# Optimization experiments

Measured on AMD Instinct MI355X. Metric: run time of the kernel, lower is better.

Reference implementation:

```python
import jax, jax.numpy as jnp
import numpy as np

N_ATOMS = 50000
N_EDGES = 500000
N_BASIS = 128
N_FILTERS = 128
N_GAUSS = 50
N_CONV = 3
CUTOFF = 5.0
MOL_SIZE = 1000


def ssp(x):
    # shifted softplus: softplus(x) - log(2)
    return jax.nn.softplus(x) - jnp.log(2.0).astype(x.dtype)


def setup_inputs() -> dict:
    key = jax.random.key(0)
    ks = jax.random.split(key, 24)

    r = jax.random.randint(ks[0], (N_ATOMS, 1), 1, 100)            # atomic numbers (0 is padding)
    xyz = jax.random.normal(ks[1], (N_ATOMS, 3)) * 3.0             # coordinates
    a = jax.random.randint(ks[2], (N_EDGES, 2), 0, N_ATOMS)        # edge list [E,2]

    embed = jax.random.normal(ks[3], (100, N_BASIS)) * 0.1
    embed = embed.at[0].set(0.0)                                   # padding_idx=0

    def w(k, fan_in, fan_out):
        return jax.random.normal(k, (fan_in, fan_out)) / jnp.sqrt(fan_in)

    def wl(k, fan_in, fan_out):  # stacked over N_CONV layers
        return jax.random.normal(k, (N_CONV, fan_in, fan_out)) / jnp.sqrt(fan_in)

    inp = {
        "r": r, "xyz": xyz, "a": a, "mol_size": MOL_SIZE,
        "embed": embed,
        # per-conv node filter Dense(B,F)
        "Wn": wl(ks[4], N_BASIS, N_FILTERS), "bn": jnp.zeros((N_CONV, N_FILTERS)),
        # per-conv edge filter Dense(G,G) -> ssp -> Dense(G,F)
        "We1": wl(ks[5], N_GAUSS, N_GAUSS), "be1": jnp.zeros((N_CONV, N_GAUSS)),
        "We2": wl(ks[6], N_GAUSS, N_FILTERS), "be2": jnp.zeros((N_CONV, N_FILTERS)),
        # per-conv update Dense(F,B) -> ssp -> Dense(B,B)
        "Wu1": wl(ks[7], N_FILTERS, N_BASIS), "bu1": jnp.zeros((N_CONV, N_BASIS)),
        "Wu2": wl(ks[8], N_BASIS, N_BASIS), "bu2": jnp.zeros((N_CONV, N_BASIS)),
        # readout
        "W1": w(ks[9], N_BASIS, N_BASIS // 2), "b1": jnp.zeros((N_BASIS // 2,)),
        "W2": w(ks[10], N_BASIS // 2, 1), "b2": jnp.zeros((1,)),
    }
    return inp


def reference(r, xyz, a, mol_size, embed, Wn, bn, We1, be1, We2, be2,
              Wu1, bu1, Wu2, bu2, W1, b1, W2, b2):
    n = xyz.shape[0]
    i, j = a[:, 0], a[:, 1]

    # per-edge distances [E,1]
    d = jnp.sqrt(jnp.sum((xyz[i] - xyz[j]) ** 2, axis=1, keepdims=True))

    # Gaussian smearing (fixed, non-trainable): offsets linspace(0, cutoff, G)
    offsets = jnp.linspace(0.0, CUTOFF, N_GAUSS)
    width = offsets[1] - offsets[0]
    coeff = -0.5 / (width ** 2)
    g = jnp.exp(coeff * (d - offsets[None, :]) ** 2)  # [E, G]

    # atom embedding [n, B]
    h = embed[r[:, 0]]

    for l in range(N_CONV):
        ef = ssp(g @ We1[l] + be1[l]) @ We2[l] + be2[l]          # [E, F] edge filter
        nodef = h @ Wn[l] + bn[l]                                # [n, F] node filter
        # symmetric message passing over undirected edge list
        agg = jax.ops.segment_sum(nodef[j] * ef, i, num_segments=n) \
            + jax.ops.segment_sum(nodef[i] * ef, j, num_segments=n)  # [n, F]
        dr = ssp(agg @ Wu1[l] + bu1[l]) @ Wu2[l] + bu2[l]        # [n, B]
        h = h + dr

    # atomwise readout
    e_atom = ssp(h @ W1 + b1) @ W2 + b2                          # [n, 1]

    # per-molecule pooling (equal-size molecules)
    seg = jnp.arange(n) // mol_size
    return jax.ops.segment_sum(e_atom, seg, num_segments=n // mol_size)  # [n_mols, 1]
```

## Files before the change

### kernel.cpp

```cpp
#include <hip/hip_runtime.h>
#include <hip/hip_bf16.h>

#define NG 50
#define NB 128

__device__ __forceinline__ float sspf(float x){
  float t = __expf(-fabsf(x));
  return fmaxf(x, 0.f) + __logf(1.f + t) - 0.6931471805599453094f;
}

constexpr float RBF_STEP  = 5.0f / 49.0f;
constexpr float RBF_COEFF = -0.5f / (RBF_STEP * RBF_STEP);

__global__ void embed_k(const int* __restrict__ r, const float* __restrict__ embed,
                        float* __restrict__ h, int N){
  int idx = blockIdx.x * blockDim.x + threadIdx.x;
  if (idx < N * 32){
    int n = idx >> 5, c = (idx & 31) * 4;
    *(float4*)&h[(size_t)n * NB + c] = *(const float4*)&embed[(size_t)r[n] * NB + c];
  }
}

__global__ void dist_k(const int* __restrict__ a, const float* __restrict__ xyz,
                       float* __restrict__ d, int E){
  int e = blockIdx.x * blockDim.x + threadIdx.x;
  if (e < E){
    int i = a[2*e], j = a[2*e+1];
    float dx = xyz[3*i+0] - xyz[3*j+0];
    float dy = xyz[3*i+1] - xyz[3*j+1];
    float dz = xyz[3*i+2] - xyz[3*j+2];
    d[e] = sqrtf(dx*dx + dy*dy + dz*dz);
  }
}

__global__ void hist_k(const int* __restrict__ a, int* __restrict__ cnt, int E){
  int e = blockIdx.x * blockDim.x + threadIdx.x;
  if (e < E){
    atomicAdd(&cnt[a[2*e]],   1);
    atomicAdd(&cnt[a[2*e+1]], 1);
  }
}

__global__ void pad_k(const int* __restrict__ cnt, int* __restrict__ pcnt, int N){
  int i = blockIdx.x*blockDim.x + threadIdx.x;
  if (i < N) pcnt[i] = (cnt[i] + 7) & ~7;
}

#define SCAN_TILE 512
__global__ void reduce_k(const int* __restrict__ cnt, int* __restrict__ bsum, int N){
  __shared__ int s[256];
  int b = blockIdx.x, t = threadIdx.x;
  int i0 = b*SCAN_TILE + t;
  int v = 0;
  if (i0 < N)       v += cnt[i0];
  if (i0+256 < N)   v += cnt[i0+256];
  s[t] = v; __syncthreads();
  for (int o=128;o>0;o>>=1){ if (t<o) s[t]+=s[t+o]; __syncthreads(); }
  if (t==0) bsum[b] = s[0];
}

__global__ void scanb_k(const int* __restrict__ bsum, int* __restrict__ boff, int nb){
  if (threadIdx.x==0 && blockIdx.x==0){
    int acc = 0;
    for (int i=0;i<nb;i++){ boff[i]=acc; acc+=bsum[i]; }
  }
}

__global__ void scan2_k(const int* __restrict__ cnt, const int* __restrict__ boff,
                        int* __restrict__ rowptr, int N, int total){
  __shared__ int s[256];
  int b = blockIdx.x, t = threadIdx.x;
  int i0 = b*SCAN_TILE;
  int a0 = (i0+2*t   < N) ? cnt[i0+2*t]   : 0;
  int a1 = (i0+2*t+1 < N) ? cnt[i0+2*t+1] : 0;
  int pair = a0 + a1;
  s[t] = pair; __syncthreads();
  for (int o=1;o<256;o<<=1){
    int v = (t>=o) ? s[t-o] : 0;
    __syncthreads();
    s[t] += v;
    __syncthreads();
  }
  int excl = s[t] - pair + boff[b];
  if (i0+2*t   < N) rowptr[i0+2*t]   = excl;
  if (i0+2*t+1 < N) rowptr[i0+2*t+1] = excl + a0;
  if (b==0 && t==0) rowptr[N] = total;
}

__global__ void copy_k(const int* __restrict__ src, int* __restrict__ dst, int n){
  int i = blockIdx.x*blockDim.x + threadIdx.x;
  if (i < n) dst[i] = src[i];
}

__global__ void fill_k(const int* __restrict__ a, int* __restrict__ cur,
                       int* __restrict__ asrc, int* __restrict__ aedg,
                       int* __restrict__ tgtv, int E){
  int e = blockIdx.x*blockDim.x + threadIdx.x;
  if (e < E){
    int i = a[2*e], j = a[2*e+1];
    int p = atomicAdd(&cur[i], 1);
    asrc[p] = j; aedg[p] = e; tgtv[p] = i;
    int q = atomicAdd(&cur[j], 1);
    asrc[q] = i; aedg[q] = e; tgtv[q] = j;
  }
}

template<int ACT, int RESID>
__launch_bounds__(128, 3)
__global__ void gemm128_k(const float* __restrict__ in, const float* __restrict__ W,
                          const float* __restrict__ bias, float* __restrict__ out, int N){
  __shared__ float As[32][64];
  __shared__ float Ws[32][128];
  int tid = threadIdx.x;
  int tc = tid & 15, tr = tid >> 4;
  int row0 = blockIdx.x * 64;
  int c0 = tc * 8;

  float bcol[8];
  {
    float4 b0 = *(const float4*)&bias[c0];
    float4 b1 = *(const float4*)&bias[c0+4];
    bcol[0]=b0.x; bcol[1]=b0.y; bcol[2]=b0.z; bcol[3]=b0.w;
    bcol[4]=b1.x; bcol[5]=b1.y; bcol[6]=b1.z; bcol[7]=b1.w;
  }
  float acc[8][8];
  #pragma unroll
  for (int r=0;r<8;r++)
    #pragma unroll
    for (int q=0;q<8;q++) acc[r][q] = bcol[q];

  for (int kc=0; kc<4; kc++){
    #pragma unroll
    for (int p=0;p<4;p++){
      int f = tid + 128*p;
      int rr = f >> 3, kq = f & 7;
      int grow = row0 + rr;
      float4 v = (grow < N) ? *(const float4*)&in[(size_t)grow*NB + kc*32 + kq*4]
                            : make_float4(0.f,0.f,0.f,0.f);
      As[kq*4+0][rr] = v.x; As[kq*4+1][rr] = v.y;
      As[kq*4+2][rr] = v.z; As[kq*4+3][rr] = v.w;
    }
    #pragma unroll
    for (int p=0;p<8;p++){
      int f = tid + 128*p;
      int wk = f >> 5, cq = f & 31;
      *(float4*)&Ws[wk][cq*4] = *(const float4*)&W[(size_t)(kc*32+wk)*NB + cq*4];
    }
    __syncthreads();
    #pragma unroll 4
    for (int k=0;k<32;k++){
      float4 a0 = *(const float4*)&As[k][tr*8];
      float4 a1 = *(const float4*)&As[k][tr*8+4];
      float4 w0 = *(const float4*)&Ws[k][c0];
      float4 w1 = *(const float4*)&Ws[k][c0+4];
      float av[8] = {a0.x,a0.y,a0.z,a0.w,a1.x,a1.y,a1.z,a1.w};
      float wv[8] = {w0.x,w0.y,w0.z,w0.w,w1.x,w1.y,w1.z,w1.w};
      #pragma unroll
      for (int r=0;r<8;r++)
        #pragma unroll
        for (int q=0;q<8;q++) acc[r][q] += av[r]*wv[q];
    }
    __syncthreads();
  }
  #pragma unroll
  for (int r=0;r<8;r++){
    int row = row0 + tr*8 + r;
    if (row < N){
      float v[8];
      #pragma unroll
      for (int q=0;q<8;q++) v[q] = (ACT==1) ? sspf(acc[r][q]) : acc[r][q];
      if (RESID){
        float4 o0 = *(const float4*)&out[(size_t)row*NB + c0];
        float4 o1 = *(const float4*)&out[(size_t)row*NB + c0+4];
        v[0]+=o0.x; v[1]+=o0.y; v[2]+=o0.z; v[3]+=o0.w;
        v[4]+=o1.x; v[5]+=o1.y; v[6]+=o1.z; v[7]+=o1.w;
      }
      *(float4*)&out[(size_t)row*NB + c0]   = make_float4(v[0],v[1],v[2],v[3]);
      *(float4*)&out[(size_t)row*NB + c0+4] = make_float4(v[4],v[5],v[6],v[7]);
    }
  }
}

__launch_bounds__(256, 2)
__global__ void visit2_k(const float* __restrict__ dists,
                         const int* __restrict__ asrc, const int* __restrict__ aedg,
                         const int* __restrict__ tgtv,
                         const float* __restrict__ nodef,
                         const float* __restrict__ We1, const float* __restrict__ be1,
                         const float* __restrict__ We2, const float* __restrict__ be2,
                         float* __restrict__ agg, int Vmax){
  __shared__ float We1s[NG][64];
  __shared__ float We2s[NG][NB];
  __shared__ float buf[NG][NB];
  __shared__ float be1s[64], be2s[NB];
  __shared__ float ds_[NB];
  __shared__ int   srcs[NB], tgts[NB];
  __shared__ int   tgt8[16];
  int tid = threadIdx.x;

  int vbase = blockIdx.x * NB;
  if (tid < NB){
    int p = vbase + tid;
    if (p < Vmax){
      srcs[tid] = asrc[p]; tgts[tid] = tgtv[p];
      ds_[tid]  = dists[aedg[p]];
    } else {
      srcs[tid] = 0; tgts[tid] = -1; ds_[tid] = 0.f;
    }
  }
  __syncthreads();
  if (tgts[0] < 0) return;

  for (int idx = tid; idx < NG*64; idx += 256){
    int m = idx >> 6, k = idx & 63;
    We1s[m][k] = (k < NG) ? We1[m*NG + k] : 0.f;
  }
  for (int idx = tid; idx < NG*NB; idx += 256)
    We2s[0][idx] = We2[idx];
  if (tid < 64)  be1s[tid] = (tid < NG) ? be1[tid] : 0.f;
  if (tid < NB)  be2s[tid] = be2[tid];
  if (tid < 16)  tgt8[tid] = tgts[tid*8];

  for (int idx = tid; idx < NG*NB; idx += 256){
    int m = idx >> 7, e = idx & 127;
    float t = ds_[e] - RBF_STEP * (float)m;
    buf[m][e] = __expf(RBF_COEFF * t * t);
  }
  __syncthreads();

  int te = tid >> 4, tk = tid & 15;
  int e0 = te * 8, k0 = tk * 4;

  float tacc[8][4];
  {
    float4 bv = *(const float4*)&be1s[k0];
    float bq[4] = {bv.x,bv.y,bv.z,bv.w};
    #pragma unroll
    for (int r=0;r<8;r++)
      #pragma unroll
      for (int q=0;q<4;q++) tacc[r][q] = bq[q];
  }
  #pragma unroll 2
  for (int m=0;m<NG;m++){
    float4 w  = *(const float4*)&We1s[m][k0];
    float4 g0 = *(const float4*)&buf[m][e0];
    float4 g1 = *(const float4*)&buf[m][e0+4];
    float ge[8] = {g0.x,g0.y,g0.z,g0.w,g1.x,g1.y,g1.z,g1.w};
    float wv[4] = {w.x,w.y,w.z,w.w};
    #pragma unroll
    for (int r=0;r<8;r++)
      #pragma unroll
      for (int q=0;q<4;q++) tacc[r][q] += ge[r]*wv[q];
  }
  __syncthreads();
  #pragma unroll
  for (int q=0;q<4;q++){
    int k = k0 + q;
    if (k < NG){
      float v[8];
      #pragma unroll
      for (int r=0;r<8;r++) v[r] = sspf(tacc[r][q]);
      *(float4*)&buf[k][e0]   = make_float4(v[0],v[1],v[2],v[3]);
      *(float4*)&buf[k][e0+4] = make_float4(v[4],v[5],v[6],v[7]);
    }
  }
  __syncthreads();

  int c0 = tk * 8;
  float acc[8][8];
  {
    float4 b0 = *(const float4*)&be2s[c0];
    float4 b1 = *(const float4*)&be2s[c0+4];
    float bq[8] = {b0.x,b0.y,b0.z,b0.w,b1.x,b1.y,b1.z,b1.w};
    #pragma unroll
    for (int r=0;r<8;r++)
      #pragma unroll
      for (int q=0;q<8;q++) acc[r][q] = bq[q];
  }
  #pragma unroll 2
  for (int k=0;k<NG;k++){
    float4 w0 = *(const float4*)&We2s[k][c0];
    float4 w1 = *(const float4*)&We2s[k][c0+4];
    float4 t0 = *(const float4*)&buf[k][e0];
    float4 t1 = *(const float4*)&buf[k][e0+4];
    float tv[8] = {t0.x,t0.y,t0.z,t0.w,t1.x,t1.y,t1.z,t1.w};
    float wv[8] = {w0.x,w0.y,w0.z,w0.w,w1.x,w1.y,w1.z,w1.w};
    #pragma unroll
    for (int r=0;r<8;r++)
      #pragma unroll
      for (int q=0;q<8;q++) acc[r][q] += tv[r]*wv[q];
  }
  __syncthreads();

  float run[8];
  #pragma unroll
  for (int q=0;q<8;q++) run[q] = 0.f;
  #pragma unroll
  for (int r=0;r<8;r++){
    int t = tgts[e0+r];
    int s = srcs[e0+r];
    float4 n0 = *(const float4*)&nodef[(size_t)s*NB + c0];
    float4 n1 = *(const float4*)&nodef[(size_t)s*NB + c0+4];
    float nv[8] = {n0.x,n0.y,n0.z,n0.w,n1.x,n1.y,n1.z,n1.w};
    if (t >= 0){
      #pragma unroll
      for (int q=0;q<8;q++) run[q] += acc[r][q] * nv[q];
    }
  }
  float* part = &buf[0][0];
  #pragma unroll
  for (int q=0;q<8;q++) part[te*NB + c0 + q] = run[q];
  __syncthreads();

  int g = te;
  int t = tgt8[g];
  if (t >= 0 && (g == 0 || tgt8[g-1] != t)){
    int gend = g;
    while (gend+1 < 16 && tgt8[gend+1] == t) gend++;
    float s[8];
    #pragma unroll
    for (int q=0;q<8;q++) s[q] = 0.f;
    for (int g2=g; g2<=gend; ++g2)
      #pragma unroll
      for (int q=0;q<8;q++) s[q] += part[g2*NB + c0 + q];
    float* ap = &agg[(size_t)t*NB + c0];
    bool border = (g == 0) || (gend == 15);
    if (border){
      #pragma unroll
      for (int q=0;q<8;q++) atomicAdd(ap+q, s[q]);
    } else {
      *(float4*)ap     = make_float4(s[0],s[1],s[2],s[3]);
      *(float4*)(ap+4) = make_float4(s[4],s[5],s[6],s[7]);
    }
  }
}

__launch_bounds__(256, 2)
__global__ void visit_k(const float* __restrict__ dists,
                        const int* __restrict__ asrc, const int* __restrict__ aedg,
                        const int* __restrict__ tgtv,
                        const float* __restrict__ nodef,
                        const float* __restrict__ We1, const float* __restrict__ be1,
                        const float* __restrict__ We2, const float* __restrict__ be2,
                        float* __restrict__ agg, int V){
  __shared__ float We1s[NG][64];
  __shared__ float We2s[NG][NB];
  __shared__ float buf[NG][NB];
  __shared__ float be1s[64], be2s[NB];
  __shared__ float ds_[NB];
  __shared__ int   srcs[NB], tgts[NB];
  int tid = threadIdx.x;

  for (int idx = tid; idx < NG*64; idx += 256){
    int m = idx >> 6, k = idx & 63;
    We1s[m][k] = (k < NG) ? We1[m*NG + k] : 0.f;
  }
  for (int idx = tid; idx < NG*NB; idx += 256)
    We2s[0][idx] = We2[idx];
  if (tid < 64)  be1s[tid] = (tid < NG) ? be1[tid] : 0.f;
  if (tid < NB)  be2s[tid] = be2[tid];

  int vbase = blockIdx.x * NB;
  if (tid < NB){
    int p = vbase + tid;
    if (p < V){
      srcs[tid] = asrc[p]; tgts[tid] = tgtv[p];
      ds_[tid]  = dists[aedg[p]];
    } else {
      srcs[tid] = 0; tgts[tid] = -1; ds_[tid] = 0.f;
    }
  }
  __syncthreads();
  for (int idx = tid; idx < NG*NB; idx += 256){
    int m = idx >> 7, e = idx & 127;
    float t = ds_[e] - RBF_STEP * (float)m;
    buf[m][e] = __expf(RBF_COEFF * t * t);
  }
  __syncthreads();
  int te = tid >> 4, tk = tid & 15;
  int e0 = te * 8, k0 = tk * 4;
  float tacc[8][4];
  {
    float4 bv = *(const float4*)&be1s[k0];
    float bq[4] = {bv.x,bv.y,bv.z,bv.w};
    #pragma unroll
    for (int r=0;r<8;r++)
      #pragma unroll
      for (int q=0;q<4;q++) tacc[r][q] = bq[q];
  }
  #pragma unroll 2
  for (int m=0;m<NG;m++){
    float4 w  = *(const float4*)&We1s[m][k0];
    float4 g0 = *(const float4*)&buf[m][e0];
    float4 g1 = *(const float4*)&buf[m][e0+4];
    float ge[8] = {g0.x,g0.y,g0.z,g0.w,g1.x,g1.y,g1.z,g1.w};
    float wv[4] = {w.x,w.y,w.z,w.w};
    #pragma unroll
    for (int r=0;r<8;r++)
      #pragma unroll
      for (int q=0;q<4;q++) tacc[r][q] += ge[r]*wv[q];
  }
  __syncthreads();
  #pragma unroll
  for (int q=0;q<4;q++){
    int k = k0 + q;
    if (k < NG){
      float v[8];
      #pragma unroll
      for (int r=0;r<8;r++) v[r] = sspf(tacc[r][q]);
      *(float4*)&buf[k][e0]   = make_float4(v[0],v[1],v[2],v[3]);
      *(float4*)&buf[k][e0+4] = make_float4(v[4],v[5],v[6],v[7]);
    }
  }
  __syncthreads();
  int c0 = tk * 8;
  float acc[8][8];
  {
    float4 b0 = *(const float4*)&be2s[c0];
    float4 b1 = *(const float4*)&be2s[c0+4];
    float bq[8] = {b0.x,b0.y,b0.z,b0.w,b1.x,b1.y,b1.z,b1.w};
    #pragma unroll
    for (int r=0;r<8;r++)
      #pragma unroll
      for (int q=0;q<8;q++) acc[r][q] = bq[q];
  }
  #pragma unroll 2
  for (int k=0;k<NG;k++){
    float4 w0 = *(const float4*)&We2s[k][c0];
    float4 w1 = *(const float4*)&We2s[k][c0+4];
    float4 t0 = *(const float4*)&buf[k][e0];
    float4 t1 = *(const float4*)&buf[k][e0+4];
    float tv[8] = {t0.x,t0.y,t0.z,t0.w,t1.x,t1.y,t1.z,t1.w};
    float wv[8] = {w0.x,w0.y,w0.z,w0.w,w1.x,w1.y,w1.z,w1.w};
    #pragma unroll
    for (int r=0;r<8;r++)
      #pragma unroll
      for (int q=0;q<8;q++) acc[r][q] += tv[r]*wv[q];
  }
  int   curtgt = tgts[e0];
  float run[8];
  #pragma unroll
  for (int q=0;q<8;q++) run[q] = 0.f;
  #pragma unroll
  for (int r=0;r<8;r++){
    int t = tgts[e0+r];
    int s = srcs[e0+r];
    float4 n0 = *(const float4*)&nodef[(size_t)s*NB + c0];
    float4 n1 = *(const float4*)&nodef[(size_t)s*NB + c0+4];
    float nv[8] = {n0.x,n0.y,n0.z,n0.w,n1.x,n1.y,n1.z,n1.w};
    if (t != curtgt){
      if (curtgt >= 0){
        float* ap = &agg[(size_t)curtgt*NB + c0];
        #pragma unroll
        for (int q=0;q<8;q++) atomicAdd(ap+q, run[q]);
      }
      curtgt = t;
      #pragma unroll
      for (int q=0;q<8;q++) run[q] = 0.f;
    }
    if (t >= 0){
      #pragma unroll
      for (int q=0;q<8;q++) run[q] += acc[r][q] * nv[q];
    }
  }
  if (curtgt >= 0){
    float* ap = &agg[(size_t)curtgt*NB + c0];
    #pragma unroll
    for (int q=0;q<8;q++) atomicAdd(ap+q, run[q]);
  }
}

__launch_bounds__(256, 2)
__global__ void edge_k(const float* __restrict__ dists, const int* __restrict__ a,
                       const float* __restrict__ nodef,
                       const float* __restrict__ We1, const float* __restrict__ be1,
                       const float* __restrict__ We2, const float* __restrict__ be2,
                       float* __restrict__ agg, int E){
  __shared__ float We1s[NG][64];
  __shared__ float We2s[NG][NB];
  __shared__ float buf[NG][NB];
  __shared__ float be1s[64], be2s[NB];
  __shared__ float ds_[NB];
  __shared__ int   ijs[2*NB];
  int tid = threadIdx.x;

  for (int idx = tid; idx < NG*64; idx += 256){
    int m = idx >> 6, k = idx & 63;
    We1s[m][k] = (k < NG) ? We1[m*NG + k] : 0.f;
  }
  for (int idx = tid; idx < NG*NB; idx += 256)
    We2s[0][idx] = We2[idx];
  if (tid < 64)  be1s[tid] = (tid < NG) ? be1[tid] : 0.f;
  if (tid < NB)  be2s[tid] = be2[tid];

  int ebase = blockIdx.x * NB;
  if (tid < NB){
    int e = ebase + tid;
    if (e < E){ ds_[tid] = dists[e]; ijs[2*tid] = a[2*e]; ijs[2*tid+1] = a[2*e+1]; }
    else      { ds_[tid] = 0.f;      ijs[2*tid] = -1;     ijs[2*tid+1] = -1; }
  }
  __syncthreads();
  for (int idx = tid; idx < NG*NB; idx += 256){
    int m = idx >> 7, e = idx & 127;
    float t = ds_[e] - RBF_STEP * (float)m;
    buf[m][e] = __expf(RBF_COEFF * t * t);
  }
  __syncthreads();
  int te = tid >> 4, tk = tid & 15;
  int e0 = te * 8, k0 = tk * 4;
  float tacc[8][4];
  {
    float4 bv = *(const float4*)&be1s[k0];
    float bq[4] = {bv.x,bv.y,bv.z,bv.w};
    #pragma unroll
    for (int r=0;r<8;r++)
      #pragma unroll
      for (int q=0;q<4;q++) tacc[r][q] = bq[q];
  }
  #pragma unroll 2
  for (int m=0;m<NG;m++){
    float4 w  = *(const float4*)&We1s[m][k0];
    float4 g0 = *(const float4*)&buf[m][e0];
    float4 g1 = *(const float4*)&buf[m][e0+4];
    float ge[8] = {g0.x,g0.y,g0.z,g0.w,g1.x,g1.y,g1.z,g1.w};
    float wv[4] = {w.x,w.y,w.z,w.w};
    #pragma unroll
    for (int r=0;r<8;r++)
      #pragma unroll
      for (int q=0;q<4;q++) tacc[r][q] += ge[r]*wv[q];
  }
  __syncthreads();
  #pragma unroll
  for (int q=0;q<4;q++){
    int k = k0 + q;
    if (k < NG){
      float v[8];
      #pragma unroll
      for (int r=0;r<8;r++) v[r] = sspf(tacc[r][q]);
      *(float4*)&buf[k][e0]   = make_float4(v[0],v[1],v[2],v[3]);
      *(float4*)&buf[k][e0+4] = make_float4(v[4],v[5],v[6],v[7]);
    }
  }
  __syncthreads();
  int c0 = tk * 8;
  float acc[8][8];
  {
    float4 b0 = *(const float4*)&be2s[c0];
    float4 b1 = *(const float4*)&be2s[c0+4];
    float bq[8] = {b0.x,b0.y,b0.z,b0.w,b1.x,b1.y,b1.z,b1.w};
    #pragma unroll
    for (int r=0;r<8;r++)
      #pragma unroll
      for (int q=0;q<8;q++) acc[r][q] = bq[q];
  }
  #pragma unroll 2
  for (int k=0;k<NG;k++){
    float4 w0 = *(const float4*)&We2s[k][c0];
    float4 w1 = *(const float4*)&We2s[k][c0+4];
    float4 t0 = *(const float4*)&buf[k][e0];
    float4 t1 = *(const float4*)&buf[k][e0+4];
    float tv[8] = {t0.x,t0.y,t0.z,t0.w,t1.x,t1.y,t1.z,t1.w};
    float wv[8] = {w0.x,w0.y,w0.z,w0.w,w1.x,w1.y,w1.z,w1.w};
    #pragma unroll
    for (int r=0;r<8;r++)
      #pragma unroll
      for (int q=0;q<8;q++) acc[r][q] += tv[r]*wv[q];
  }
  #pragma unroll
  for (int r=0;r<8;r++){
    int el = e0 + r;
    int i = ijs[2*el], j = ijs[2*el+1];
    if (i < 0) continue;
    float4 nj0 = *(const float4*)&nodef[(size_t)j*NB + c0];
    float4 nj1 = *(const float4*)&nodef[(size_t)j*NB + c0+4];
    float4 ni0 = *(const float4*)&nodef[(size_t)i*NB + c0];
    float4 ni1 = *(const float4*)&nodef[(size_t)i*NB + c0+4];
    float* ai = &agg[(size_t)i*NB + c0];
    float* aj = &agg[(size_t)j*NB + c0];
    float njv[8] = {nj0.x,nj0.y,nj0.z,nj0.w,nj1.x,nj1.y,nj1.z,nj1.w};
    float niv[8] = {ni0.x,ni0.y,ni0.z,ni0.w,ni1.x,ni1.y,ni1.z,ni1.w};
    #pragma unroll
    for (int q=0;q<8;q++){
      atomicAdd(ai+q, njv[q]*acc[r][q]);
      atomicAdd(aj+q, niv[q]*acc[r][q]);
    }
  }
}

__launch_bounds__(128, 3)
__global__ void readout_k(const float* __restrict__ h, const float* __restrict__ W1,
                          const float* __restrict__ b1, const float* __restrict__ W2,
                          const float* __restrict__ b2, const int* __restrict__ molp,
                          float* __restrict__ out, int N){
  __shared__ float As[32][64];
  __shared__ float W1s[32][64];
  __shared__ float segsum[2];
  int tid = threadIdx.x;
  int tc = tid & 15, tr = tid >> 4;
  int row0 = blockIdx.x * 64;
  int c0 = tc * 4;

  float acc[8][4];
  {
    float4 bv = *(const float4*)&b1[c0];
    float bq[4] = {bv.x,bv.y,bv.z,bv.w};
    #pragma unroll
    for (int r=0;r<8;r++)
      #pragma unroll
      for (int q=0;q<4;q++) acc[r][q] = bq[q];
  }
  for (int kc=0;kc<4;kc++){
    #pragma unroll
    for (int p=0;p<4;p++){
      int f = tid + 128*p; int rr = f >> 3; int kq = f & 7;
      int grow = row0 + rr;
      float4 v = (grow < N) ? *(const float4*)&h[(size_t)grow*NB + kc*32 + kq*4]
                            : make_float4(0.f,0.f,0.f,0.f);
      As[kq*4+0][rr] = v.x; As[kq*4+1][rr] = v.y;
      As[kq*4+2][rr] = v.z; As[kq*4+3][rr] = v.w;
    }
    #pragma unroll
    for (int p=0;p<4;p++){
      int f = tid + 128*p; int wk = f >> 4; int cq = f & 15;
      *(float4*)&W1s[wk][cq*4] = *(const float4*)&W1[(size_t)(kc*32+wk)*64 + cq*4];
    }
    __syncthreads();
    #pragma unroll 4
    for (int k=0;k<32;k++){
      float4 a0 = *(const float4*)&As[k][tr*8];
      float4 a1 = *(const float4*)&As[k][tr*8+4];
      float4 w  = *(const float4*)&W1s[k][c0];
      float av[8] = {a0.x,a0.y,a0.z,a0.w,a1.x,a1.y,a1.z,a1.w};
      float wv[4] = {w.x,w.y,w.z,w.w};
      #pragma unroll
      for (int r=0;r<8;r++)
        #pragma unroll
        for (int q=0;q<4;q++) acc[r][q] += av[r]*wv[q];
    }
    __syncthreads();
  }
  float4 w2f = *(const float4*)&W2[c0];
  float part[8];
  #pragma unroll
  for (int r=0;r<8;r++)
    part[r] = sspf(acc[r][0])*w2f.x + sspf(acc[r][1])*w2f.y +
              sspf(acc[r][2])*w2f.z + sspf(acc[r][3])*w2f.w;
  #pragma unroll
  for (int off=1; off<16; off<<=1)
    #pragma unroll
    for (int r=0;r<8;r++) part[r] += __shfl_xor(part[r], off);

  if (tid < 2) segsum[tid] = 0.f;
  __syncthreads();
  int ms = molp[0];
  float b2v = b2[0];
  int seg0 = row0 / ms;
  if (tc == 0){
    #pragma unroll
    for (int r=0;r<8;r++){
      int row = row0 + tr*8 + r;
      if (row < N){
        int s = row/ms - seg0;
        if (s < 2) atomicAdd(&segsum[s], part[r] + b2v);
        else       atomicAdd(&out[row/ms], part[r] + b2v);
      }
    }
  }
  __syncthreads();
  if (tid == 0 && segsum[0] != 0.f) atomicAdd(&out[seg0], segsum[0]);
  if (tid == 1){
    int lastrow = row0 + 63; if (lastrow > N-1) lastrow = N-1;
    if (lastrow/ms > seg0 && segsum[1] != 0.f) atomicAdd(&out[seg0+1], segsum[1]);
  }
}

extern "C" void kernel_launch(void* const* d_in, const int* in_sizes, int n_in,
                              void* d_out, int out_size, void* d_ws, size_t ws_size,
                              hipStream_t stream){
  const int*   r     = (const int*)  d_in[0];
  const float* xyz   = (const float*)d_in[1];
  const int*   a     = (const int*)  d_in[2];
  const int*   molp  = (const int*)  d_in[3];
  const float* embed = (const float*)d_in[4];
  const float* Wn    = (const float*)d_in[5];
  const float* bn    = (const float*)d_in[6];
  const float* We1   = (const float*)d_in[7];
  const float* be1   = (const float*)d_in[8];
  const float* We2   = (const float*)d_in[9];
  const float* be2   = (const float*)d_in[10];
  const float* Wu1   = (const float*)d_in[11];
  const float* bu1   = (const float*)d_in[12];
  const float* Wu2   = (const float*)d_in[13];
  const float* bu2   = (const float*)d_in[14];
  const float* W1    = (const float*)d_in[15];
  const float* b1    = (const float*)d_in[16];
  const float* W2    = (const float*)d_in[17];
  const float* b2    = (const float*)d_in[18];

  int N = in_sizes[0];
  int E = in_sizes[2] / 2;
  int V = 2*E;
  size_t VmaxS = (size_t)V + 8*(size_t)N;

  float* ws   = (float*)d_ws;
  size_t E4   = ((size_t)E + 3) & ~(size_t)3;
  size_t NSZ  = (size_t)N * NB;
  size_t RPAD = ((size_t)N + 1 + 3) & ~(size_t)3;
  size_t NPAD = ((size_t)N + 3) & ~(size_t)3;
  size_t base = E4 + 3*NSZ;

  size_t need1 = (base + RPAD + 3*NPAD + 512 + 3*VmaxS) * sizeof(float);
  size_t need2 = (base + RPAD + 2*NPAD + 512 + 3*(size_t)V) * sizeof(float);

  float* dbuf  = ws;
  float* h     = dbuf + E4;
  float* nodef = h + NSZ;
  float* agg   = nodef + NSZ;

  int gblocks = (N + 63)/64;
  int eblocks = (E + 127)/128;
  int nb = (N + SCAN_TILE - 1) / SCAN_TILE;

  embed_k<<<(N*32 + 255)/256, 256, 0, stream>>>(r, embed, h, N);
  dist_k <<<(E + 255)/256,    256, 0, stream>>>(a, xyz, dbuf, E);

  if (ws_size >= need1){
    int* rowptr = (int*)(agg + NSZ);
    int* cnt    = rowptr + RPAD;
    int* pcnt   = cnt + NPAD;
    int* cur    = pcnt + NPAD;
    int* bsum   = cur + NPAD;
    int* boff   = bsum + 256;
    int* asrc   = boff + 256;
    int* aedg   = asrc + VmaxS;
    int* tgtv   = aedg + VmaxS;

    (void)hipMemsetAsync(cnt, 0, (size_t)N*sizeof(int), stream);
    (void)hipMemsetAsync(asrc, 0, VmaxS*sizeof(int), stream);
    (void)hipMemsetAsync(aedg, 0, VmaxS*sizeof(int), stream);
    (void)hipMemsetAsync(tgtv, 0xFF, VmaxS*sizeof(int), stream);
    hist_k  <<<(E + 255)/256, 256, 0, stream>>>(a, cnt, E);
    pad_k   <<<(N + 255)/256, 256, 0, stream>>>(cnt, pcnt, N);
    reduce_k<<<nb, 256, 0, stream>>>(pcnt, bsum, N);
    scanb_k <<<1, 64, 0, stream>>>(bsum, boff, nb);
    scan2_k <<<nb, 256, 0, stream>>>(pcnt, boff, rowptr, N, 0);
    copy_k  <<<(N + 255)/256, 256, 0, stream>>>(rowptr, cur, N);
    fill_k  <<<(E + 255)/256, 256, 0, stream>>>(a, cur, asrc, aedg, tgtv, E);

    int vblocks = (int)((VmaxS + 127)/128);
    for (int l = 0; l < 3; l++){
      gemm128_k<0,0><<<gblocks, 128, 0, stream>>>(h, Wn + (size_t)l*NB*NB, bn + l*NB, nodef, N);
      (void)hipMemsetAsync(agg, 0, NSZ*sizeof(float), stream);
      visit2_k<<<vblocks, 256, 0, stream>>>(dbuf, asrc, aedg, tgtv, nodef,
                                            We1 + (size_t)l*NG*NG, be1 + l*NG,
                                            We2 + (size_t)l*NG*NB, be2 + l*NB, agg, (int)VmaxS);
      gemm128_k<1,0><<<gblocks, 128, 0, stream>>>(agg,   Wu1 + (size_t)l*NB*NB, bu1 + l*NB, nodef, N);
      gemm128_k<0,1><<<gblocks, 128, 0, stream>>>(nodef, Wu2 + (size_t)l*NB*NB, bu2 + l*NB, h, N);
    }
  } else if (ws_size >= need2){
    int* rowptr = (int*)(agg + NSZ);
    int* cnt    = rowptr + RPAD;
    int* cur    = cnt + NPAD;
    int* bsum   = cur + NPAD;
    int* boff   = bsum + 256;
    int* asrc   = boff + 256;
    int* aedg   = asrc + V;
    int* tgtv   = aedg + V;

    (void)hipMemsetAsync(cnt, 0, (size_t)N*sizeof(int), stream);
    hist_k  <<<(E + 255)/256, 256, 0, stream>>>(a, cnt, E);
    reduce_k<<<nb, 256, 0, stream>>>(cnt, bsum, N);
    scanb_k <<<1, 64, 0, stream>>>(bsum, boff, nb);
    scan2_k <<<nb, 256, 0, stream>>>(cnt, boff, rowptr, N, V);
    copy_k  <<<(N + 255)/256, 256, 0, stream>>>(rowptr, cur, N);
    fill_k  <<<(E + 255)/256, 256, 0, stream>>>(a, cur, asrc, aedg, tgtv, E);

    int vblocks = (V + 127)/128;
    for (int l = 0; l < 3; l++){
      gemm128_k<0,0><<<gblocks, 128, 0, stream>>>(h, Wn + (size_t)l*NB*NB, bn + l*NB, nodef, N);
      (void)hipMemsetAsync(agg, 0, NSZ*sizeof(float), stream);
      visit_k<<<vblocks, 256, 0, stream>>>(dbuf, asrc, aedg, tgtv, nodef,
                                           We1 + (size_t)l*NG*NG, be1 + l*NG,
                                           We2 + (size_t)l*NG*NB, be2 + l*NB, agg, V);
      gemm128_k<1,0><<<gblocks, 128, 0, stream>>>(agg,   Wu1 + (size_t)l*NB*NB, bu1 + l*NB, nodef, N);
      gemm128_k<0,1><<<gblocks, 128, 0, stream>>>(nodef, Wu2 + (size_t)l*NB*NB, bu2 + l*NB, h, N);
    }
  } else {
    for (int l = 0; l < 3; l++){
      gemm128_k<0,0><<<gblocks, 128, 0, stream>>>(h, Wn + (size_t)l*NB*NB, bn + l*NB, nodef, N);
      (void)hipMemsetAsync(agg, 0, NSZ*sizeof(float), stream);
      edge_k<<<eblocks, 256, 0, stream>>>(dbuf, a, nodef,
                                          We1 + (size_t)l*NG*NG, be1 + l*NG,
                                          We2 + (size_t)l*NG*NB, be2 + l*NB, agg, E);
      gemm128_k<1,0><<<gblocks, 128, 0, stream>>>(agg,   Wu1 + (size_t)l*NB*NB, bu1 + l*NB, nodef, N);
      gemm128_k<0,1><<<gblocks, 128, 0, stream>>>(nodef, Wu2 + (size_t)l*NB*NB, bu2 + l*NB, h, N);
    }
  }

  (void)hipMemsetAsync(d_out, 0, (size_t)out_size*sizeof(float), stream);
  readout_k<<<gblocks, 128, 0, stream>>>(h, W1, b1, W2, b2, molp, (float*)d_out, N);
}
```

Baseline: 1.723 ms.

## Store distances per visit slot and read padded We1 from global to cut LDS

fill_k now writes each edge's distance straight into the CSR-ordered visit array, so visit kernels load it without the aedg indirection. We1 and be1 are padded once into a workspace buffer by a new padw_k kernel, and visit2_k reads them (and be2) from global memory instead of staging them in shared memory. The freed LDS lets launch bounds rise from 2 to 3 blocks per CU, trading shared-memory weight reads for cached global loads in the inner loop.

```diff
diff --git a/kernel.cpp b/kernel.cpp
--- a/kernel.cpp
+++ b/kernel.cpp
@@ -30,6 +30,19 @@
     float dy = xyz[3*i+1] - xyz[3*j+1];
     float dz = xyz[3*i+2] - xyz[3*j+2];
     d[e] = sqrtf(dx*dx + dy*dy + dz*dz);
+  }
+}
+
+__global__ void padw_k(const float* __restrict__ We1, const float* __restrict__ be1,
+                       float* __restrict__ We1p, float* __restrict__ be1p){
+  int idx = blockIdx.x*blockDim.x + threadIdx.x;
+  if (idx < 3*NG*64){
+    int l = idx/(NG*64), rem = idx%(NG*64), m = rem>>6, k = rem&63;
+    We1p[idx] = (k < NG) ? We1[((size_t)l*NG + m)*NG + k] : 0.f;
+  }
+  if (idx < 3*64){
+    int l = idx>>6, k = idx&63;
+    be1p[idx] = (k < NG) ? be1[l*NG + k] : 0.f;
   }
 }
 
@@ -92,16 +105,18 @@
   if (i < n) dst[i] = src[i];
 }
 
-__global__ void fill_k(const int* __restrict__ a, int* __restrict__ cur,
-                       int* __restrict__ asrc, int* __restrict__ aedg,
+__global__ void fill_k(const int* __restrict__ a, const float* __restrict__ dists,
+                       int* __restrict__ cur,
+                       int* __restrict__ asrc, float* __restrict__ dvis,
                        int* __restrict__ tgtv, int E){
   int e = blockIdx.x*blockDim.x + threadIdx.x;
   if (e < E){
     int i = a[2*e], j = a[2*e+1];
+    float d = dists[e];
     int p = atomicAdd(&cur[i], 1);
-    asrc[p] = j; aedg[p] = e; tgtv[p] = i;
+    asrc[p] = j; dvis[p] = d; tgtv[p] = i;
     int q = atomicAdd(&cur[j], 1);
-    asrc[q] = i; aedg[q] = e; tgtv[q] = j;
+    asrc[q] = i; dvis[q] = d; tgtv[q] = j;
   }
 }
 
@@ -181,18 +196,16 @@
   }
 }
 
-__launch_bounds__(256, 2)
-__global__ void visit2_k(const float* __restrict__ dists,
-                         const int* __restrict__ asrc, const int* __restrict__ aedg,
+__launch_bounds__(256, 3)
+__global__ void visit2_k(const float* __restrict__ dvis,
+                         const int* __restrict__ asrc,
                          const int* __restrict__ tgtv,
                          const float* __restrict__ nodef,
-                         const float* __restrict__ We1, const float* __restrict__ be1,
+                         const float* __restrict__ We1p, const float* __restrict__ be1p,
                          const float* __restrict__ We2, const float* __restrict__ be2,
                          float* __restrict__ agg, int Vmax){
-  __shared__ float We1s[NG][64];
   __shared__ float We2s[NG][NB];
   __shared__ float buf[NG][NB];
-  __shared__ float be1s[64], be2s[NB];
   __shared__ float ds_[NB];
   __shared__ int   srcs[NB], tgts[NB];
   __shared__ int   tgt8[16];
@@ -202,8 +215,7 @@
   if (tid < NB){
     int p = vbase + tid;
     if (p < Vmax){
-      srcs[tid] = asrc[p]; tgts[tid] = tgtv[p];
-      ds_[tid]  = dists[aedg[p]];
+      srcs[tid] = asrc[p]; tgts[tid] = tgtv[p]; ds_[tid] = dvis[p];
     } else {
       srcs[tid] = 0; tgts[tid] = -1; ds_[tid] = 0.f;
     }
@@ -211,14 +223,8 @@
   __syncthreads();
   if (tgts[0] < 0) return;
 
-  for (int idx = tid; idx < NG*64; idx += 256){
-    int m = idx >> 6, k = idx & 63;
-    We1s[m][k] = (k < NG) ? We1[m*NG + k] : 0.f;
-  }
   for (int idx = tid; idx < NG*NB; idx += 256)
     We2s[0][idx] = We2[idx];
-  if (tid < 64)  be1s[tid] = (tid < NG) ? be1[tid] : 0.f;
-  if (tid < NB)  be2s[tid] = be2[tid];
   if (tid < 16)  tgt8[tid] = tgts[tid*8];
 
   for (int idx = tid; idx < NG*NB; idx += 256){
@@ -233,7 +239,7 @@
 
   float tacc[8][4];
   {
-    float4 bv = *(const float4*)&be1s[k0];
+    float4 bv = *(const float4*)&be1p[k0];
     float bq[4] = {bv.x,bv.y,bv.z,bv.w};
     #pragma unroll
     for (int r=0;r<8;r++)
@@ -242,7 +248,7 @@
   }
   #pragma unroll 2
   for (int m=0;m<NG;m++){
-    float4 w  = *(const float4*)&We1s[m][k0];
+    float4 w  = *(const float4*)&We1p[m*64 + k0];
     float4 g0 = *(const float4*)&buf[m][e0];
     float4 g1 = *(const float4*)&buf[m][e0+4];
     float ge[8] = {g0.x,g0.y,g0.z,g0.w,g1.x,g1.y,g1.z,g1.w};
@@ -269,8 +275,8 @@
   int c0 = tk * 8;
   float acc[8][8];
   {
-    float4 b0 = *(const float4*)&be2s[c0];
-    float4 b1 = *(const float4*)&be2s[c0+4];
+    float4 b0 = *(const float4*)&be2[c0];
+    float4 b1 = *(const float4*)&be2[c0+4];
     float bq[8] = {b0.x,b0.y,b0.z,b0.w,b1.x,b1.y,b1.z,b1.w};
     #pragma unroll
     for (int r=0;r<8;r++)
@@ -336,8 +342,8 @@
 }
 
 __launch_bounds__(256, 2)
-__global__ void visit_k(const float* __restrict__ dists,
-                        const int* __restrict__ asrc, const int* __restrict__ aedg,
+__global__ void visit_k(const float* __restrict__ dvis,
+                        const int* __restrict__ asrc,
                         const int* __restrict__ tgtv,
                         const float* __restrict__ nodef,
                         const float* __restrict__ We1, const float* __restrict__ be1,
@@ -364,8 +370,7 @@
   if (tid < NB){
     int p = vbase + tid;
     if (p < V){
-      srcs[tid] = asrc[p]; tgts[tid] = tgtv[p];
-      ds_[tid]  = dists[aedg[p]];
+      srcs[tid] = asrc[p]; tgts[tid] = tgtv[p]; ds_[tid] = dvis[p];
     } else {
       srcs[tid] = 0; tgts[tid] = -1; ds_[tid] = 0.f;
     }
@@ -708,8 +713,9 @@
   size_t RPAD = ((size_t)N + 1 + 3) & ~(size_t)3;
   size_t NPAD = ((size_t)N + 3) & ~(size_t)3;
   size_t base = E4 + 3*NSZ;
-
-  size_t need1 = (base + RPAD + 3*NPAD + 512 + 3*VmaxS) * sizeof(float);
+  size_t WPAD = 3*NG*64 + 3*64;
+
+  size_t need1 = (base + RPAD + 3*NPAD + 512 + 3*VmaxS + WPAD) * sizeof(float);
   size_t need2 = (base + RPAD + 2*NPAD + 512 + 3*(size_t)V) * sizeof(float);
 
   float* dbuf  = ws;
@@ -725,47 +731,50 @@
   dist_k <<<(E + 255)/256,    256, 0, stream>>>(a, xyz, dbuf, E);
 
   if (ws_size >= need1){
-    int* rowptr = (int*)(agg + NSZ);
-    int* cnt    = rowptr + RPAD;
-    int* pcnt   = cnt + NPAD;
-    int* cur    = pcnt + NPAD;
-    int* bsum   = cur + NPAD;
-    int* boff   = bsum + 256;
-    int* asrc   = boff + 256;
-    int* aedg   = asrc + VmaxS;
-    int* tgtv   = aedg + VmaxS;
+    int*   rowptr = (int*)(agg + NSZ);
+    int*   cnt    = rowptr + RPAD;
+    int*   pcnt   = cnt + NPAD;
+    int*   cur    = pcnt + NPAD;
+    int*   bsum   = cur + NPAD;
+    int*   boff   = bsum + 256;
+    int*   asrc   = boff + 256;
+    int*   tgtv   = asrc + VmaxS;
+    float* dvis   = (float*)(tgtv + VmaxS);
+    float* We1p   = dvis + VmaxS;
+    float* be1p   = We1p + 3*NG*64;
 
     (void)hipMemsetAsync(cnt, 0, (size_t)N*sizeof(int), stream);
     (void)hipMemsetAsync(asrc, 0, VmaxS*sizeof(int), stream);
-    (void)hipMemsetAsync(aedg, 0, VmaxS*sizeof(int), stream);
     (void)hipMemsetAsync(tgtv, 0xFF, VmaxS*sizeof(int), stream);
+    (void)hipMemsetAsync(dvis, 0, VmaxS*sizeof(float), stream);
+    padw_k  <<<(3*NG*64 + 255)/256, 256, 0, stream>>>(We1, be1, We1p, be1p);
     hist_k  <<<(E + 255)/256, 256, 0, stream>>>(a, cnt, E);
     pad_k   <<<(N + 255)/256, 256, 0, stream>>>(cnt, pcnt, N);
     reduce_k<<<nb, 256, 0, stream>>>(pcnt, bsum, N);
     scanb_k <<<1, 64, 0, stream>>>(bsum, boff, nb);
     scan2_k <<<nb, 256, 0, stream>>>(pcnt, boff, rowptr, N, 0);
     copy_k  <<<(N + 255)/256, 256, 0, stream>>>(rowptr, cur, N);
-    fill_k  <<<(E + 255)/256, 256, 0, stream>>>(a, cur, asrc, aedg, tgtv, E);
+    fill_k  <<<(E + 255)/256, 256, 0, stream>>>(a, dbuf, cur, asrc, dvis, tgtv, E);
 
     int vblocks = (int)((VmaxS + 127)/128);
     for (int l = 0; l < 3; l++){
       gemm128_k<0,0><<<gblocks, 128, 0, stream>>>(h, Wn + (size_t)l*NB*NB, bn + l*NB, nodef, N);
       (void)hipMemsetAsync(agg, 0, NSZ*sizeof(float), stream);
-      visit2_k<<<vblocks, 256, 0, stream>>>(dbuf, asrc, aedg, tgtv, nodef,
-                                            We1 + (size_t)l*NG*NG, be1 + l*NG,
+      visit2_k<<<vblocks, 256, 0, stream>>>(dvis, asrc, tgtv, nodef,
+                                            We1p + (size_t)l*NG*64, be1p + (size_t)l*64,
                                             We2 + (size_t)l*NG*NB, be2 + l*NB, agg, (int)VmaxS);
       gemm128_k<1,0><<<gblocks, 128, 0, stream>>>(agg,   Wu1 + (size_t)l*NB*NB, bu1 + l*NB, nodef, N);
       gemm128_k<0,1><<<gblocks, 128, 0, stream>>>(nodef, Wu2 + (size_t)l*NB*NB, bu2 + l*NB, h, N);
     }
   } else if (ws_size >= need2){
-    int* rowptr = (int*)(agg + NSZ);
-    int* cnt    = rowptr + RPAD;
-    int* cur    = cnt + NPAD;
-    int* bsum   = cur + NPAD;
-    int* boff   = bsum + 256;
-    int* asrc   = boff + 256;
-    int* aedg   = asrc + V;
-    int* tgtv   = aedg + V;
+    int*   rowptr = (int*)(agg + NSZ);
+    int*   cnt    = rowptr + RPAD;
+    int*   cur    = cnt + NPAD;
+    int*   bsum   = cur + NPAD;
+    int*   boff   = bsum + 256;
+    int*   asrc   = boff + 256;
+    int*   tgtv   = asrc + V;
+    float* dvis   = (float*)(tgtv + V);
 
     (void)hipMemsetAsync(cnt, 0, (size_t)N*sizeof(int), stream);
     hist_k  <<<(E + 255)/256, 256, 0, stream>>>(a, cnt, E);
@@ -773,13 +782,13 @@
     scanb_k <<<1, 64, 0, stream>>>(bsum, boff, nb);
     scan2_k <<<nb, 256, 0, stream>>>(cnt, boff, rowptr, N, V);
     copy_k  <<<(N + 255)/256, 256, 0, stream>>>(rowptr, cur, N);
-    fill_k  <<<(E + 255)/256, 256, 0, stream>>>(a, cur, asrc, aedg, tgtv, E);
+    fill_k  <<<(E + 255)/256, 256, 0, stream>>>(a, dbuf, cur, asrc, dvis, tgtv, E);
 
     int vblocks = (V + 127)/128;
     for (int l = 0; l < 3; l++){
       gemm128_k<0,0><<<gblocks, 128, 0, stream>>>(h, Wn + (size_t)l*NB*NB, bn + l*NB, nodef, N);
       (void)hipMemsetAsync(agg, 0, NSZ*sizeof(float), stream);
-      visit_k<<<vblocks, 256, 0, stream>>>(dbuf, asrc, aedg, tgtv, nodef,
+      visit_k<<<vblocks, 256, 0, stream>>>(dvis, asrc, tgtv, nodef,
                                            We1 + (size_t)l*NG*NG, be1 + l*NG,
                                            We2 + (size_t)l*NG*NB, be2 + l*NB, agg, V);
       gemm128_k<1,0><<<gblocks, 128, 0, stream>>>(agg,   Wu1 + (size_t)l*NB*NB, bu1 + l*NB, nodef, N);
```

Measured after the change: 1.551 ms. -10.0%, faster.
